# Optimization experiments

Measured on AMD Instinct MI355X. Metric: run time of the kernel, lower is better.

The kernel has to match this reference:

```python
import jax, jax.numpy as jnp
import numpy as np

B, L, H, HEADS = 2, 2048, 1024, 16
D = H // HEADS  # head_dim = 64


def _rel_pos_bias(q, pos_emb):
    """Skewing trick: q is (b,h,L,d) (already scaled), pos_emb is (2L-1,d).
    Returns relative positional bias of shape (b,h,L,L)."""
    b, h, l, _ = q.shape
    p = jnp.einsum('bhid,jd->bhij', q, pos_emb)          # (b,h,L,2L-1)
    p = jnp.pad(p, ((0, 0), (0, 0), (0, 0), (0, 1)))     # (b,h,L,2L)
    p = p.reshape(b, h, l * 2 * l)                        # flatten last two dims
    p = jnp.pad(p, ((0, 0), (0, 0), (0, l - 1)))          # append L-1 zeros
    p = p.reshape(b, h, l + 1, 2 * l - 1)
    return p[:, :, :-1, -l:]                              # (b,h,L,L)


def setup_inputs() -> dict:
    key = jax.random.key(0)
    ks = jax.random.split(key, 12)
    s = 1.0 / np.sqrt(H)
    inp = {
        'query': jax.random.normal(ks[0], (B, L, H), jnp.float32),
        'key':   jax.random.normal(ks[1], (B, L, H), jnp.float32),
        'value': jax.random.normal(ks[2], (B, L, H), jnp.float32),
        'Wq_w': jax.random.normal(ks[3], (H, H), jnp.float32) * s,
        'Wq_b': jnp.zeros((H,), jnp.float32),
        'Wk_w': jax.random.normal(ks[4], (H, H), jnp.float32) * s,
        'Wk_b': jnp.zeros((H,), jnp.float32),
        'Wv_w': jax.random.normal(ks[5], (H, H), jnp.float32) * s,
        'Wv_b': jnp.zeros((H,), jnp.float32),
        'Wo_w': jax.random.normal(ks[6], (H, H), jnp.float32) * s,
        'Wo_b': jnp.zeros((H,), jnp.float32),
        'pos_emb': jax.random.normal(ks[7], (2 * L - 1, D), jnp.float32),
    }
    return inp


def reference(query, key, value, Wq_w, Wq_b, Wk_w, Wk_b, Wv_w, Wv_b, Wo_w, Wo_b, pos_emb):
    b = query.shape[0]
    q = query @ Wq_w.T + Wq_b
    k = key @ Wk_w.T + Wk_b
    v = value @ Wv_w.T + Wv_b
    # (b,L,h*d) -> (b,h,L,d)
    split = lambda x: x.reshape(b, L, HEADS, D).transpose(0, 2, 1, 3)
    q, k, v = split(q), split(k), split(v)
    q = q / np.sqrt(D)  # note: scaled q is also used for positional bias (faithful)
    attn = jnp.einsum('bhid,bhjd->bhij', q, k)
    attn = attn + _rel_pos_bias(q, pos_emb)
    causal = jnp.triu(jnp.full((L, L), -jnp.inf, jnp.float32), k=1)
    attn = attn + causal  # broadcasts over (b,h)
    score = jax.nn.softmax(attn, axis=-1)
    out = jnp.einsum('bhqk,bhkd->bhqd', score, v)
    out = out.transpose(0, 2, 1, 3).reshape(b, L, H)
    return out @ Wo_w.T + Wo_b
```

## Files before the change

kernel.cpp:

```cpp
#include <hip/hip_runtime.h>

#define L_SEQ 2048
#define NH    16
#define HD    64
#define HDIM  1024

typedef __attribute__((ext_vector_type(8))) short  short8;
typedef __attribute__((ext_vector_type(4))) float  f32x4;

__device__ __forceinline__ unsigned short f2bf(float f) {
    unsigned int u = __float_as_uint(f);
    u += 0x7fffu + ((u >> 16) & 1u);
    return (unsigned short)(u >> 16);
}

__device__ __forceinline__ short8 ld8(const unsigned short* p) {
    return *(const short8*)p;
}

__device__ __forceinline__ unsigned int cvtpk(float a, float b) {
    unsigned int r;
    asm("v_cvt_pk_bf16_f32 %0, %1, %2" : "=v"(r) : "v"(a), "v"(b));
    return r;
}

__device__ __forceinline__ void gl16(const unsigned short* g, unsigned short* l) {
    __builtin_amdgcn_global_load_lds(
        (const __attribute__((address_space(1))) void*)g,
        (__attribute__((address_space(3))) void*)l, 16, 0, 0);
}

__global__ __launch_bounds__(256) void cvt_a_kernel(
    const float* __restrict__ q, const float* __restrict__ k, const float* __restrict__ v,
    const float* __restrict__ Wq, const float* __restrict__ Wk,
    const float* __restrict__ Wv, const float* __restrict__ Wo,
    const float* __restrict__ pe,
    unsigned short* __restrict__ S1, unsigned short* __restrict__ Vb,
    unsigned short* __restrict__ VSCR,
    unsigned short* __restrict__ D, unsigned short* __restrict__ E)
{
    const int y = blockIdx.y;
    const float* src; unsigned short* dst; int n8;
    switch (y) {
        case 0:  src = q;  dst = S1;            n8 = 524288; break;
        case 1:  src = k;  dst = Vb;            n8 = 524288; break;
        case 2:  src = Wq; dst = D;             n8 = 131072; break;
        case 3:  src = Wk; dst = D + 1048576;   n8 = 131072; break;
        case 4:  src = Wv; dst = D + 2097152;   n8 = 131072; break;
        case 5:  src = Wo; dst = D + 3145728;   n8 = 131072; break;
        case 6:  src = pe; dst = E;             n8 = 32760;  break;
        default: src = v;  dst = VSCR;          n8 = 524288; break;
    }
    const int i = blockIdx.x * 256 + threadIdx.x;
    if (i >= n8) return;
    const float4 a = ((const float4*)src)[2 * i];
    const float4 b = ((const float4*)src)[2 * i + 1];
    union { short8 v; unsigned int u[4]; } o;
    o.u[0] = cvtpk(a.x, a.y); o.u[1] = cvtpk(a.z, a.w);
    o.u[2] = cvtpk(b.x, b.y); o.u[3] = cvtpk(b.z, b.w);
    ((short8*)dst)[i] = o.v;
}

__device__ __forceinline__ void gemm_bf16_core(
    const unsigned short* __restrict__ Xb,
    const unsigned short* __restrict__ Wb,
    int row0, int col0,
    unsigned short* As, unsigned short* Bs,
    f32x4 (&acc)[4][4])
{
    const int t    = threadIdx.x;
    const int lane = t & 63;
    const int wid  = t >> 6;
    const int lr   = lane & 15;
    const int lg   = lane >> 4;
    const int wr   = (wid >> 1) << 6;
    const int wc   = (wid & 1) << 6;

    const int grow = lane >> 3;
    const int gcol = ((lane & 7) ^ grow) << 3;

#pragma unroll
    for (int m = 0; m < 4; ++m)
#pragma unroll
        for (int n = 0; n < 4; ++n)
            acc[m][n] = (f32x4)0.0f;

    const unsigned short* xs = Xb + (size_t)(row0 + grow) * 1024 + gcol;
    const unsigned short* ws = Wb + (size_t)(col0 + grow) * 1024 + gcol;

    for (int k0 = 0; k0 < 1024; k0 += 64) {
        __syncthreads();
#pragma unroll
        for (int i = 0; i < 4; ++i) {
            const int seg = (i << 2) + wid;
            gl16(xs + (size_t)(seg << 3) * 1024 + k0, As + seg * 512);
            gl16(ws + (size_t)(seg << 3) * 1024 + k0, Bs + seg * 512);
        }
        __syncthreads();

        short8 af[4][2], bf[4][2];
#pragma unroll
        for (int m = 0; m < 4; ++m) {
            const int row = wr + (m << 4) + lr;
#pragma unroll
            for (int h = 0; h < 2; ++h)
                af[m][h] = ld8(&As[row * 64 + ((((h << 2) + lg) ^ (lr & 7)) << 3)]);
        }
#pragma unroll
        for (int n = 0; n < 4; ++n) {
            const int row = wc + (n << 4) + lr;
#pragma unroll
            for (int h = 0; h < 2; ++h)
                bf[n][h] = ld8(&Bs[row * 64 + ((((h << 2) + lg) ^ (lr & 7)) << 3)]);
        }
#pragma unroll
        for (int m = 0; m < 4; ++m)
#pragma unroll
            for (int n = 0; n < 4; ++n) {
                acc[m][n] = __builtin_amdgcn_mfma_f32_16x16x32_bf16(af[m][0], bf[n][0], acc[m][n], 0, 0, 0);
                acc[m][n] = __builtin_amdgcn_mfma_f32_16x16x32_bf16(af[m][1], bf[n][1], acc[m][n], 0, 0, 0);
            }
    }
}

__global__ __launch_bounds__(256) void proj_qkv_kernel(
    const unsigned short* __restrict__ Xq, const unsigned short* __restrict__ Xk,
    const unsigned short* __restrict__ Xv, const unsigned short* __restrict__ D,
    const float* __restrict__ bq, const float* __restrict__ bk, const float* __restrict__ bv,
    unsigned short* __restrict__ Qb, unsigned short* __restrict__ Kb,
    unsigned short* __restrict__ VT)
{
    __shared__ __align__(16) unsigned short As[128 * 64];
    __shared__ __align__(16) unsigned short Bs[128 * 64];

    const int z = blockIdx.x >> 8;
    const int d = blockIdx.x & 255;
    const int y = ((d >> 6) << 3) | (d & 7);
    const int x = (d >> 3) & 7;
    const int row0 = y << 7, col0 = x << 7;

    const unsigned short* Xb = (z == 0) ? Xq : (z == 1) ? Xk : Xv;
    const unsigned short* Wb = D + (size_t)z * 1048576;
    const float* bias = (z == 0) ? bq : (z == 1) ? bk : bv;

    f32x4 acc[4][4];
    gemm_bf16_core(Xb, Wb, row0, col0, As, Bs, acc);

    const int t = threadIdx.x;
    const int lane = t & 63;
    const int wid  = t >> 6;
    const int lr = lane & 15, lg = lane >> 4;
    const int wr = (wid >> 1) << 6, wc = (wid & 1) << 6;

    if (z <= 1) {
        const float scale = (z == 0) ? 0.125f * 1.44269504088896340736f : 1.0f;
        unsigned short* out = (z == 0) ? Qb : Kb;
#pragma unroll
        for (int n = 0; n < 4; ++n) {
            const int o = col0 + wc + (n << 4) + lr;
            const float bo = bias[o];
            const int h = o >> 6, dd = o & 63;
#pragma unroll
            for (int m = 0; m < 4; ++m) {
                const int ib = row0 + wr + (m << 4) + (lg << 2);
#pragma unroll
                for (int r = 0; r < 4; ++r) {
                    const int i = ib + r;
                    out[(((size_t)((i >> 11) * NH + h)) * L_SEQ + (i & (L_SEQ - 1))) * HD + dd] =
                        f2bf((acc[m][n][r] + bo) * scale);
                }
            }
        }
    } else {
#pragma unroll
        for (int n = 0; n < 4; ++n) {
            const int o = col0 + wc + (n << 4) + lr;
            const float bo = bias[o];
            const int h = o >> 6, dd = o & 63;
#pragma unroll
            for (int m = 0; m < 4; ++m) {
                const int ib = row0 + wr + (m << 4) + (lg << 2);
                const int b = ib >> 11, il = ib & (L_SEQ - 1);
                ushort4 pk;
                pk.x = f2bf(acc[m][n][0] + bo);
                pk.y = f2bf(acc[m][n][1] + bo);
                pk.z = f2bf(acc[m][n][2] + bo);
                pk.w = f2bf(acc[m][n][3] + bo);
                *(ushort4*)&VT[(((size_t)(b * NH + h)) * HD + dd) * L_SEQ + il] = pk;
            }
        }
    }
}

__global__ __launch_bounds__(256) void outproj_kernel(
    const unsigned short* __restrict__ Ob, const unsigned short* __restrict__ Wb,
    const float* __restrict__ bias, float* __restrict__ Yout)
{
    __shared__ __align__(16) unsigned short As[128 * 64];
    __shared__ __align__(16) unsigned short Bs[128 * 64];

    const int d = blockIdx.x;
    const int y = ((d >> 6) << 3) | (d & 7);
    const int x = (d >> 3) & 7;
    const int row0 = y << 7, col0 = x << 7;

    f32x4 acc[4][4];
    gemm_bf16_core(Ob, Wb, row0, col0, As, Bs, acc);

    const int t = threadIdx.x;
    const int lane = t & 63;
    const int wid  = t >> 6;
    const int lr = lane & 15, lg = lane >> 4;
    const int wr = (wid >> 1) << 6, wc = (wid & 1) << 6;

#pragma unroll
    for (int n = 0; n < 4; ++n) {
        const int o = col0 + wc + (n << 4) + lr;
        const float bo = bias[o];
#pragma unroll
        for (int m = 0; m < 4; ++m) {
            const int ib = row0 + wr + (m << 4) + (lg << 2);
#pragma unroll
            for (int r = 0; r < 4; ++r)
                Yout[(size_t)(ib + r) * HDIM + o] = acc[m][n][r] + bo;
        }
    }
}

__device__ __forceinline__ void stage_kv(
    const unsigned short* __restrict__ kbase, const unsigned short* __restrict__ vbase,
    int j0, unsigned short (*Ksb)[64], unsigned short (*Vsb)[64], int wid, int lane)
{
    const int r8 = lane >> 3;
    const int gc = ((lane & 7) ^ r8) << 3;
#pragma unroll
    for (int s = 0; s < 2; ++s) {
        const int rw = (wid << 4) + (s << 3);
        gl16(kbase + (size_t)(j0 + rw + r8) * HD + gc, &Ksb[rw][0]);
        gl16(vbase + (size_t)(rw + r8) * L_SEQ + j0 + gc, &Vsb[rw][0]);
    }
}

__global__ __launch_bounds__(256, 3) void attn_kernel(
    const unsigned short* __restrict__ Q,
    const unsigned short* __restrict__ Kt,
    const unsigned short* __restrict__ VT,
    const unsigned short* __restrict__ PE,
    unsigned short* __restrict__ O)
{
    __shared__ __align__(16) unsigned short Ks[2][64][64];
    __shared__ __align__(16) unsigned short Vs[2][64][64];
    __shared__ __align__(16) float blds_all[4][64][20];

    const int t    = threadIdx.x;
    const int wid  = t >> 6;
    const int lane = t & 63;
    const int lr   = lane & 15;
    const int lg   = lane >> 4;
    const int lk   = lg << 3;

    const int p   = blockIdx.x;
    const int bh  = p & 31;
    const int rb  = 31 - (p >> 5);
    const int i0  = rb << 6;
    const int i0w = i0 + (wid << 4);
    const int nt  = rb + 1;

    const unsigned short* kbase = Kt + (size_t)bh * L_SEQ * HD;
    const unsigned short* vbase = VT + (size_t)bh * HD * L_SEQ;

    float (*blds)[20] = blds_all[wid];

    const unsigned short* qb = Q + ((size_t)bh * L_SEQ + i0w + lr) * HD + lk;
    const short8 aq0 = ld8(qb);
    const short8 aq1 = ld8(qb + 32);

    const int gi    = i0w + lr;
    const int idx0  = ((lg & 1) << 7) + (lr << 2);
    const int idx1  = idx0 + 64;
    const int selhi = lg >> 1;

    f32x4 oacc[4];
#pragma unroll
    for (int dt = 0; dt < 4; ++dt) oacc[dt] = (f32x4)0.0f;
    float mrun = -__builtin_inff();
    float lrun = 0.0f;

    const int jend = i0w + 15;

    f32x4 pqc = (f32x4)0.0f;
    {
        const unsigned short* pp = PE + (size_t)(2032 - i0w + lr) * HD + lk;
        pqc = __builtin_amdgcn_mfma_f32_16x16x32_bf16(aq0, ld8(pp), pqc, 0, 0, 0);
        pqc = __builtin_amdgcn_mfma_f32_16x16x32_bf16(aq1, ld8(pp + 32), pqc, 0, 0, 0);
    }

    stage_kv(kbase, vbase, 0, Ks[0], Vs[0], wid, lane);
    __syncthreads();

    int cur = 0;
    for (int tt = 0; tt < nt; ++tt) {
        const int j0   = tt << 6;
        const bool more = (tt + 1 < nt);

        if (more)
            stage_kv(kbase, vbase, j0 + 64, Ks[cur ^ 1], Vs[cur ^ 1], wid, lane);

        if (j0 <= jend) {
            f32x4 s2[4];
#pragma unroll
            for (int ct = 0; ct < 4; ++ct) {
                const int row = (ct << 4) + lr;
                const short8 k0 = *(const short8*)&Ks[cur][row][(lg ^ (lr & 7)) << 3];
                const short8 k1 = *(const short8*)&Ks[cur][row][((4 + lg) ^ (lr & 7)) << 3];
                f32x4 a = (f32x4)0.0f;
                a = __builtin_amdgcn_mfma_f32_16x16x32_bf16(k0, aq0, a, 0, 0, 0);
                a = __builtin_amdgcn_mfma_f32_16x16x32_bf16(k1, aq1, a, 0, 0, 0);
                s2[ct] = a;
            }

            const int mlo = 2032 + j0 - i0w;
            f32x4 pq[5];
            pq[0] = pqc;
#pragma unroll
            for (int pt = 1; pt < 5; ++pt) {
                f32x4 a = (f32x4)0.0f;
                const unsigned short* pp = PE + (size_t)(mlo + (pt << 4) + lr) * HD + lk;
                a = __builtin_amdgcn_mfma_f32_16x16x32_bf16(aq0, ld8(pp), a, 0, 0, 0);
                a = __builtin_amdgcn_mfma_f32_16x16x32_bf16(aq1, ld8(pp + 32), a, 0, 0, 0);
                pq[pt] = a;
            }
            pqc = pq[4];

#pragma unroll
            for (int r = 0; r < 4; ++r) {
                const int qw = (lg << 2) + r;
                {
                    const int kr = lr + qw - 15;
                    if (kr >= 0) blds[kr][qw] = pq[0][r];
                }
#pragma unroll
                for (int pt = 1; pt < 4; ++pt)
                    blds[(pt << 4) + lr + qw - 15][qw] = pq[pt][r];
                {
                    const int kr = 49 + lr + qw;
                    if (kr < 64) blds[kr][qw] = pq[4][r];
                }
            }

            if (j0 + 63 > i0w) {
#pragma unroll
                for (int ct = 0; ct < 4; ++ct)
#pragma unroll
                    for (int r = 0; r < 4; ++r) {
                        const int krl = (ct << 4) + (lg << 2) + r;
                        const float v = s2[ct][r] + blds[krl][lr];
                        s2[ct][r] = (j0 + krl > gi) ? -__builtin_inff() : v;
                    }
            } else {
#pragma unroll
                for (int ct = 0; ct < 4; ++ct)
#pragma unroll
                    for (int r = 0; r < 4; ++r) {
                        const int krl = (ct << 4) + (lg << 2) + r;
                        s2[ct][r] += blds[krl][lr];
                    }
            }

            float c0 = fmaxf(fmaxf(s2[0][0], s2[0][1]), fmaxf(s2[0][2], s2[0][3]));
            float c1 = fmaxf(fmaxf(s2[1][0], s2[1][1]), fmaxf(s2[1][2], s2[1][3]));
            float c2 = fmaxf(fmaxf(s2[2][0], s2[2][1]), fmaxf(s2[2][2], s2[2][3]));
            float c3 = fmaxf(fmaxf(s2[3][0], s2[3][1]), fmaxf(s2[3][2], s2[3][3]));
            float vmax = fmaxf(fmaxf(c0, c1), fmaxf(c2, c3));
            vmax = fmaxf(vmax, __shfl_xor(vmax, 16));
            vmax = fmaxf(vmax, __shfl_xor(vmax, 32));
            if (!__all(vmax <= mrun + 8.0f)) {
                const float mnew = fmaxf(mrun, vmax);
                const float sc = __builtin_amdgcn_exp2f(mrun - mnew);
                mrun = mnew;
                lrun *= sc;
#pragma unroll
                for (int dt = 0; dt < 4; ++dt)
#pragma unroll
                    for (int r = 0; r < 4; ++r)
                        oacc[dt][r] *= sc;
            }
#pragma unroll
            for (int ct = 0; ct < 4; ++ct)
#pragma unroll
                for (int r = 0; r < 4; ++r)
                    s2[ct][r] = __builtin_amdgcn_exp2f(s2[ct][r] - mrun);
            float t0 = (s2[0][0] + s2[0][1]) + (s2[0][2] + s2[0][3]);
            float t1 = (s2[1][0] + s2[1][1]) + (s2[1][2] + s2[1][3]);
            float t2 = (s2[2][0] + s2[2][1]) + (s2[2][2] + s2[2][3]);
            float t3 = (s2[3][0] + s2[3][1]) + (s2[3][2] + s2[3][3]);
            float sum = (t0 + t1) + (t2 + t3);
            sum += __shfl_xor(sum, 16);
            sum += __shfl_xor(sum, 32);
            lrun += sum;

            unsigned int pkl[4], pkh[4];
#pragma unroll
            for (int ct = 0; ct < 4; ++ct) {
                pkl[ct] = cvtpk(s2[ct][0], s2[ct][1]);
                pkh[ct] = cvtpk(s2[ct][2], s2[ct][3]);
            }
            union { short8 v; int u[4]; } pf0, pf1;
#pragma unroll
            for (int m = 0; m < 4; ++m) {
                const int bidx = (m & 2) ? idx1 : idx0;
                const int a0 = __builtin_amdgcn_ds_bpermute(bidx, (int)((m & 1) ? pkh[0] : pkl[0]));
                const int a1 = __builtin_amdgcn_ds_bpermute(bidx, (int)((m & 1) ? pkh[1] : pkl[1]));
                pf0.u[m] = selhi ? a1 : a0;
                const int b0 = __builtin_amdgcn_ds_bpermute(bidx, (int)((m & 1) ? pkh[2] : pkl[2]));
                const int b1 = __builtin_amdgcn_ds_bpermute(bidx, (int)((m & 1) ? pkh[3] : pkl[3]));
                pf1.u[m] = selhi ? b1 : b0;
            }

#pragma unroll
            for (int dt = 0; dt < 4; ++dt) {
                const int row = (dt << 4) + lr;
                const short8 v0 = *(const short8*)&Vs[cur][row][(lg ^ (lr & 7)) << 3];
                const short8 v1 = *(const short8*)&Vs[cur][row][((4 + lg) ^ (lr & 7)) << 3];
                oacc[dt] = __builtin_amdgcn_mfma_f32_16x16x32_bf16(v0, pf0.v, oacc[dt], 0, 0, 0);
                oacc[dt] = __builtin_amdgcn_mfma_f32_16x16x32_bf16(v1, pf1.v, oacc[dt], 0, 0, 0);
            }
        }

        __syncthreads();
        cur ^= 1;
    }

    const float inv = 1.0f / lrun;
    const int b = bh >> 4, h = bh & 15;
#pragma unroll
    for (int dt = 0; dt < 4; ++dt) {
        uint2 u;
        u.x = cvtpk(oacc[dt][0] * inv, oacc[dt][1] * inv);
        u.y = cvtpk(oacc[dt][2] * inv, oacc[dt][3] * inv);
        *(uint2*)&O[((size_t)b * L_SEQ + i0w + lr) * HDIM + (h << 6) + (dt << 4) + (lg << 2)] = u;
    }
}

extern "C" void kernel_launch(void* const* d_in, const int* in_sizes, int n_in,
                              void* d_out, int out_size, void* d_ws, size_t ws_size,
                              hipStream_t stream) {
    (void)in_sizes; (void)n_in; (void)out_size;

    const float* query   = (const float*)d_in[0];
    const float* key_    = (const float*)d_in[1];
    const float* value   = (const float*)d_in[2];
    const float* Wq_w    = (const float*)d_in[3];
    const float* Wq_b    = (const float*)d_in[4];
    const float* Wk_w    = (const float*)d_in[5];
    const float* Wk_b    = (const float*)d_in[6];
    const float* Wv_w    = (const float*)d_in[7];
    const float* Wv_b    = (const float*)d_in[8];
    const float* Wo_w    = (const float*)d_in[9];
    const float* Wo_b    = (const float*)d_in[10];
    const float* pos_emb = (const float*)d_in[11];

    char* ws = (char*)d_ws;
    const size_t MB = 1024 * 1024;
    unsigned short* S1 = (unsigned short*)(ws);
    unsigned short* Qb = (unsigned short*)(ws + 8  * MB);
    unsigned short* Kb = (unsigned short*)(ws + 16 * MB);
    unsigned short* Vb = (unsigned short*)(ws + 24 * MB);
    unsigned short* D  = (unsigned short*)(ws + 32 * MB);
    unsigned short* E  = (unsigned short*)(ws + 40 * MB);

    unsigned short* VSCR = (unsigned short*)d_out;
    unsigned short* VT   = VSCR + 4194304;

    const int npe = (2 * L_SEQ - 1) * HD;
    if (ws_size < (size_t)40 * MB + (size_t)npe * 2) return;

    cvt_a_kernel<<<dim3(2048, 8), 256, 0, stream>>>(query, key_, value,
                                                    Wq_w, Wk_w, Wv_w, Wo_w, pos_emb,
                                                    S1, Vb, VSCR, D, E);
    proj_qkv_kernel<<<768, 256, 0, stream>>>(S1, Vb, VSCR, D, Wq_b, Wk_b, Wv_b,
                                             Qb, Kb, VT);
    attn_kernel<<<1024, 256, 0, stream>>>(Qb, Kb, VT, E, S1);
    outproj_kernel<<<256, 256, 0, stream>>>(S1, D + 3145728, Wo_b, (float*)d_out);
}
```

Before: 172.1 us.

## Fuse fp32-to-bf16 activation conversion into QKV projection GEMM loads

The separate conversion pass for the query/key/value activations is removed. The QKV projection now reads fp32 activations directly, converts them to bf16 in registers and writes them into swizzled LDS, while weights still come in through async global-to-LDS loads. This avoids writing and re-reading about 24 MB of bf16 intermediates and shrinks the conversion launch to weights and pos_emb only. In exchange, each GEMM tile reads twice the activation bytes through registers synchronously, which loses the async load path and could stall the MFMA loop.

New measurement: 195.4 us. 13.5% more time.

```diff
diff --git a/kernel.cpp b/kernel.cpp
--- a/kernel.cpp
+++ b/kernel.cpp
@@ -30,27 +30,16 @@
         (__attribute__((address_space(3))) void*)l, 16, 0, 0);
 }
 
-__global__ __launch_bounds__(256) void cvt_a_kernel(
-    const float* __restrict__ q, const float* __restrict__ k, const float* __restrict__ v,
+__global__ __launch_bounds__(256) void cvt_w_kernel(
     const float* __restrict__ Wq, const float* __restrict__ Wk,
     const float* __restrict__ Wv, const float* __restrict__ Wo,
     const float* __restrict__ pe,
-    unsigned short* __restrict__ S1, unsigned short* __restrict__ Vb,
-    unsigned short* __restrict__ VSCR,
     unsigned short* __restrict__ D, unsigned short* __restrict__ E)
 {
     const int y = blockIdx.y;
-    const float* src; unsigned short* dst; int n8;
-    switch (y) {
-        case 0:  src = q;  dst = S1;            n8 = 524288; break;
-        case 1:  src = k;  dst = Vb;            n8 = 524288; break;
-        case 2:  src = Wq; dst = D;             n8 = 131072; break;
-        case 3:  src = Wk; dst = D + 1048576;   n8 = 131072; break;
-        case 4:  src = Wv; dst = D + 2097152;   n8 = 131072; break;
-        case 5:  src = Wo; dst = D + 3145728;   n8 = 131072; break;
-        case 6:  src = pe; dst = E;             n8 = 32760;  break;
-        default: src = v;  dst = VSCR;          n8 = 524288; break;
-    }
+    const float* src = (y == 0) ? Wq : (y == 1) ? Wk : (y == 2) ? Wv : (y == 3) ? Wo : pe;
+    unsigned short* dst = (y < 4) ? (D + (size_t)y * 1048576) : E;
+    const int n8 = (y < 4) ? 131072 : 32760;
     const int i = blockIdx.x * 256 + threadIdx.x;
     if (i >= n8) return;
     const float4 a = ((const float4*)src)[2 * i];
@@ -61,8 +50,8 @@
     ((short8*)dst)[i] = o.v;
 }
 
-__device__ __forceinline__ void gemm_bf16_core(
-    const unsigned short* __restrict__ Xb,
+__device__ __forceinline__ void gemm_f32x_core(
+    const float* __restrict__ Xf,
     const unsigned short* __restrict__ Wb,
     int row0, int col0,
     unsigned short* As, unsigned short* Bs,
@@ -78,6 +67,85 @@
 
     const int grow = lane >> 3;
     const int gcol = ((lane & 7) ^ grow) << 3;
+    const unsigned short* ws = Wb + (size_t)(col0 + grow) * 1024 + gcol;
+
+    const int xr  = t >> 1;
+    const int xh  = t & 1;
+    const int xsw = xr & 7;
+    const float* xs = Xf + (size_t)(row0 + xr) * 1024 + (xh << 5);
+    unsigned short* xdst = As + xr * 64;
+
+#pragma unroll
+    for (int m = 0; m < 4; ++m)
+#pragma unroll
+        for (int n = 0; n < 4; ++n)
+            acc[m][n] = (f32x4)0.0f;
+
+    for (int k0 = 0; k0 < 1024; k0 += 64) {
+        __syncthreads();
+        float4 xv[8];
+#pragma unroll
+        for (int j = 0; j < 8; ++j)
+            xv[j] = *(const float4*)(xs + k0 + 4 * j);
+#pragma unroll
+        for (int i = 0; i < 4; ++i) {
+            const int seg = (i << 2) + wid;
+            gl16(ws + (size_t)(seg << 3) * 1024 + k0, Bs + seg * 512);
+        }
+#pragma unroll
+        for (int cc = 0; cc < 4; ++cc) {
+            union { short8 v; unsigned int u[4]; } o;
+            o.u[0] = cvtpk(xv[2 * cc].x,     xv[2 * cc].y);
+            o.u[1] = cvtpk(xv[2 * cc].z,     xv[2 * cc].w);
+            o.u[2] = cvtpk(xv[2 * cc + 1].x, xv[2 * cc + 1].y);
+            o.u[3] = cvtpk(xv[2 * cc + 1].z, xv[2 * cc + 1].w);
+            const int c = (xh << 2) + cc;
+            *(short8*)(xdst + ((c ^ xsw) << 3)) = o.v;
+        }
+        __syncthreads();
+
+        short8 af[4][2], bf[4][2];
+#pragma unroll
+        for (int m = 0; m < 4; ++m) {
+            const int row = wr + (m << 4) + lr;
+#pragma unroll
+            for (int h = 0; h < 2; ++h)
+                af[m][h] = ld8(&As[row * 64 + ((((h << 2) + lg) ^ (lr & 7)) << 3)]);
+        }
+#pragma unroll
+        for (int n = 0; n < 4; ++n) {
+            const int row = wc + (n << 4) + lr;
+#pragma unroll
+            for (int h = 0; h < 2; ++h)
+                bf[n][h] = ld8(&Bs[row * 64 + ((((h << 2) + lg) ^ (lr & 7)) << 3)]);
+        }
+#pragma unroll
+        for (int m = 0; m < 4; ++m)
+#pragma unroll
+            for (int n = 0; n < 4; ++n) {
+                acc[m][n] = __builtin_amdgcn_mfma_f32_16x16x32_bf16(af[m][0], bf[n][0], acc[m][n], 0, 0, 0);
+                acc[m][n] = __builtin_amdgcn_mfma_f32_16x16x32_bf16(af[m][1], bf[n][1], acc[m][n], 0, 0, 0);
+            }
+    }
+}
+
+__device__ __forceinline__ void gemm_bf16_core(
+    const unsigned short* __restrict__ Xb,
+    const unsigned short* __restrict__ Wb,
+    int row0, int col0,
+    unsigned short* As, unsigned short* Bs,
+    f32x4 (&acc)[4][4])
+{
+    const int t    = threadIdx.x;
+    const int lane = t & 63;
+    const int wid  = t >> 6;
+    const int lr   = lane & 15;
+    const int lg   = lane >> 4;
+    const int wr   = (wid >> 1) << 6;
+    const int wc   = (wid & 1) << 6;
+
+    const int grow = lane >> 3;
+    const int gcol = ((lane & 7) ^ grow) << 3;
 
 #pragma unroll
     for (int m = 0; m < 4; ++m)
@@ -124,8 +192,8 @@
 }
 
 __global__ __launch_bounds__(256) void proj_qkv_kernel(
-    const unsigned short* __restrict__ Xq, const unsigned short* __restrict__ Xk,
-    const unsigned short* __restrict__ Xv, const unsigned short* __restrict__ D,
+    const float* __restrict__ Xq, const float* __restrict__ Xk,
+    const float* __restrict__ Xv, const unsigned short* __restrict__ D,
     const float* __restrict__ bq, const float* __restrict__ bk, const float* __restrict__ bv,
     unsigned short* __restrict__ Qb, unsigned short* __restrict__ Kb,
     unsigned short* __restrict__ VT)
@@ -139,12 +207,12 @@
     const int x = (d >> 3) & 7;
     const int row0 = y << 7, col0 = x << 7;
 
-    const unsigned short* Xb = (z == 0) ? Xq : (z == 1) ? Xk : Xv;
+    const float* Xf = (z == 0) ? Xq : (z == 1) ? Xk : Xv;
     const unsigned short* Wb = D + (size_t)z * 1048576;
     const float* bias = (z == 0) ? bq : (z == 1) ? bk : bv;
 
     f32x4 acc[4][4];
-    gemm_bf16_core(Xb, Wb, row0, col0, As, Bs, acc);
+    gemm_f32x_core(Xf, Wb, row0, col0, As, Bs, acc);
 
     const int t = threadIdx.x;
     const int lane = t & 63;
@@ -465,20 +533,16 @@
     unsigned short* S1 = (unsigned short*)(ws);
     unsigned short* Qb = (unsigned short*)(ws + 8  * MB);
     unsigned short* Kb = (unsigned short*)(ws + 16 * MB);
-    unsigned short* Vb = (unsigned short*)(ws + 24 * MB);
-    unsigned short* D  = (unsigned short*)(ws + 32 * MB);
-    unsigned short* E  = (unsigned short*)(ws + 40 * MB);
-
-    unsigned short* VSCR = (unsigned short*)d_out;
-    unsigned short* VT   = VSCR + 4194304;
+    unsigned short* D  = (unsigned short*)(ws + 24 * MB);
+    unsigned short* E  = (unsigned short*)(ws + 32 * MB);
+
+    unsigned short* VT = (unsigned short*)d_out;
 
     const int npe = (2 * L_SEQ - 1) * HD;
-    if (ws_size < (size_t)40 * MB + (size_t)npe * 2) return;
-
-    cvt_a_kernel<<<dim3(2048, 8), 256, 0, stream>>>(query, key_, value,
-                                                    Wq_w, Wk_w, Wv_w, Wo_w, pos_emb,
-                                                    S1, Vb, VSCR, D, E);
-    proj_qkv_kernel<<<768, 256, 0, stream>>>(S1, Vb, VSCR, D, Wq_b, Wk_b, Wv_b,
+    if (ws_size < (size_t)32 * MB + (size_t)npe * 2) return;
+
+    cvt_w_kernel<<<dim3(512, 5), 256, 0, stream>>>(Wq_w, Wk_w, Wv_w, Wo_w, pos_emb, D, E);
+    proj_qkv_kernel<<<768, 256, 0, stream>>>(query, key_, value, D, Wq_b, Wk_b, Wv_b,
                                              Qb, Kb, VT);
     attn_kernel<<<1024, 256, 0, stream>>>(Qb, Kb, VT, E, S1);
     outproj_kernel<<<256, 256, 0, stream>>>(S1, D + 3145728, Wo_b, (float*)d_out);
```

## Prefetch next tile's positional-bias MFMAs and raise wave priority around MFMA blocks

Applied to the files above, without the earlier changes.

Computes the positional-bias MFMA tiles for the next KV tile one iteration ahead, so their global PE loads overlap the current softmax work. The per-wave `j0 <= jend` guard is dropped, so every wave processes every tile up to nt. Also wraps the QK and PV MFMA blocks with s_setprio to favour matrix issue. The trade-off is more registers from holding two sets of five accumulators, plus redundant work on tiles that are fully masked if nt exceeds a wave's range.

Measured after the change: 187.9 us. 9.2% more time.

```diff
diff --git a/kernel.cpp b/kernel.cpp
--- a/kernel.cpp
+++ b/kernel.cpp
@@ -286,13 +286,17 @@
     float mrun = -__builtin_inff();
     float lrun = 0.0f;
 
-    const int jend = i0w + 15;
-
-    f32x4 pqc = (f32x4)0.0f;
+    f32x4 pqv[5];
     {
-        const unsigned short* pp = PE + (size_t)(2032 - i0w + lr) * HD + lk;
-        pqc = __builtin_amdgcn_mfma_f32_16x16x32_bf16(aq0, ld8(pp), pqc, 0, 0, 0);
-        pqc = __builtin_amdgcn_mfma_f32_16x16x32_bf16(aq1, ld8(pp + 32), pqc, 0, 0, 0);
+        const int m0 = 2032 - i0w;
+#pragma unroll
+        for (int pt = 0; pt < 5; ++pt) {
+            f32x4 a = (f32x4)0.0f;
+            const unsigned short* pp = PE + (size_t)(m0 + (pt << 4) + lr) * HD + lk;
+            a = __builtin_amdgcn_mfma_f32_16x16x32_bf16(aq0, ld8(pp), a, 0, 0, 0);
+            a = __builtin_amdgcn_mfma_f32_16x16x32_bf16(aq1, ld8(pp + 32), a, 0, 0, 0);
+            pqv[pt] = a;
+        }
     }
 
     stage_kv(kbase, vbase, 0, Ks[0], Vs[0], wid, lane);
@@ -306,125 +310,133 @@
         if (more)
             stage_kv(kbase, vbase, j0 + 64, Ks[cur ^ 1], Vs[cur ^ 1], wid, lane);
 
-        if (j0 <= jend) {
-            f32x4 s2[4];
-#pragma unroll
-            for (int ct = 0; ct < 4; ++ct) {
-                const int row = (ct << 4) + lr;
-                const short8 k0 = *(const short8*)&Ks[cur][row][(lg ^ (lr & 7)) << 3];
-                const short8 k1 = *(const short8*)&Ks[cur][row][((4 + lg) ^ (lr & 7)) << 3];
-                f32x4 a = (f32x4)0.0f;
-                a = __builtin_amdgcn_mfma_f32_16x16x32_bf16(k0, aq0, a, 0, 0, 0);
-                a = __builtin_amdgcn_mfma_f32_16x16x32_bf16(k1, aq1, a, 0, 0, 0);
-                s2[ct] = a;
-            }
-
-            const int mlo = 2032 + j0 - i0w;
-            f32x4 pq[5];
-            pq[0] = pqc;
+        f32x4 s2[4];
+        __builtin_amdgcn_s_setprio(1);
+#pragma unroll
+        for (int ct = 0; ct < 4; ++ct) {
+            const int row = (ct << 4) + lr;
+            const short8 k0 = *(const short8*)&Ks[cur][row][(lg ^ (lr & 7)) << 3];
+            const short8 k1 = *(const short8*)&Ks[cur][row][((4 + lg) ^ (lr & 7)) << 3];
+            f32x4 a = (f32x4)0.0f;
+            a = __builtin_amdgcn_mfma_f32_16x16x32_bf16(k0, aq0, a, 0, 0, 0);
+            a = __builtin_amdgcn_mfma_f32_16x16x32_bf16(k1, aq1, a, 0, 0, 0);
+            s2[ct] = a;
+        }
+        __builtin_amdgcn_s_setprio(0);
+
+#pragma unroll
+        for (int r = 0; r < 4; ++r) {
+            const int qw = (lg << 2) + r;
+            {
+                const int kr = lr + qw - 15;
+                if (kr >= 0) blds[kr][qw] = pqv[0][r];
+            }
+#pragma unroll
+            for (int pt = 1; pt < 4; ++pt)
+                blds[(pt << 4) + lr + qw - 15][qw] = pqv[pt][r];
+            {
+                const int kr = 49 + lr + qw;
+                if (kr < 64) blds[kr][qw] = pqv[4][r];
+            }
+        }
+
+        f32x4 pqn[5];
+        if (more) {
+            pqn[0] = pqv[4];
+            const int mlon = 2032 + j0 + 64 - i0w;
 #pragma unroll
             for (int pt = 1; pt < 5; ++pt) {
                 f32x4 a = (f32x4)0.0f;
-                const unsigned short* pp = PE + (size_t)(mlo + (pt << 4) + lr) * HD + lk;
+                const unsigned short* pp = PE + (size_t)(mlon + (pt << 4) + lr) * HD + lk;
                 a = __builtin_amdgcn_mfma_f32_16x16x32_bf16(aq0, ld8(pp), a, 0, 0, 0);
                 a = __builtin_amdgcn_mfma_f32_16x16x32_bf16(aq1, ld8(pp + 32), a, 0, 0, 0);
-                pq[pt] = a;
-            }
-            pqc = pq[4];
-
-#pragma unroll
-            for (int r = 0; r < 4; ++r) {
-                const int qw = (lg << 2) + r;
-                {
-                    const int kr = lr + qw - 15;
-                    if (kr >= 0) blds[kr][qw] = pq[0][r];
+                pqn[pt] = a;
+            }
+        }
+
+        if (j0 + 63 > i0w) {
+#pragma unroll
+            for (int ct = 0; ct < 4; ++ct)
+#pragma unroll
+                for (int r = 0; r < 4; ++r) {
+                    const int krl = (ct << 4) + (lg << 2) + r;
+                    const float v = s2[ct][r] + blds[krl][lr];
+                    s2[ct][r] = (j0 + krl > gi) ? -__builtin_inff() : v;
                 }
-#pragma unroll
-                for (int pt = 1; pt < 4; ++pt)
-                    blds[(pt << 4) + lr + qw - 15][qw] = pq[pt][r];
-                {
-                    const int kr = 49 + lr + qw;
-                    if (kr < 64) blds[kr][qw] = pq[4][r];
+        } else {
+#pragma unroll
+            for (int ct = 0; ct < 4; ++ct)
+#pragma unroll
+                for (int r = 0; r < 4; ++r) {
+                    const int krl = (ct << 4) + (lg << 2) + r;
+                    s2[ct][r] += blds[krl][lr];
                 }
-            }
-
-            if (j0 + 63 > i0w) {
-#pragma unroll
-                for (int ct = 0; ct < 4; ++ct)
-#pragma unroll
-                    for (int r = 0; r < 4; ++r) {
-                        const int krl = (ct << 4) + (lg << 2) + r;
-                        const float v = s2[ct][r] + blds[krl][lr];
-                        s2[ct][r] = (j0 + krl > gi) ? -__builtin_inff() : v;
-                    }
-            } else {
-#pragma unroll
-                for (int ct = 0; ct < 4; ++ct)
-#pragma unroll
-                    for (int r = 0; r < 4; ++r) {
-                        const int krl = (ct << 4) + (lg << 2) + r;
-                        s2[ct][r] += blds[krl][lr];
-                    }
-            }
-
-            float c0 = fmaxf(fmaxf(s2[0][0], s2[0][1]), fmaxf(s2[0][2], s2[0][3]));
-            float c1 = fmaxf(fmaxf(s2[1][0], s2[1][1]), fmaxf(s2[1][2], s2[1][3]));
-            float c2 = fmaxf(fmaxf(s2[2][0], s2[2][1]), fmaxf(s2[2][2], s2[2][3]));
-            float c3 = fmaxf(fmaxf(s2[3][0], s2[3][1]), fmaxf(s2[3][2], s2[3][3]));
-            float vmax = fmaxf(fmaxf(c0, c1), fmaxf(c2, c3));
-            vmax = fmaxf(vmax, __shfl_xor(vmax, 16));
-            vmax = fmaxf(vmax, __shfl_xor(vmax, 32));
-            if (!__all(vmax <= mrun + 8.0f)) {
-                const float mnew = fmaxf(mrun, vmax);
-                const float sc = __builtin_amdgcn_exp2f(mrun - mnew);
-                mrun = mnew;
-                lrun *= sc;
-#pragma unroll
-                for (int dt = 0; dt < 4; ++dt)
-#pragma unroll
-                    for (int r = 0; r < 4; ++r)
-                        oacc[dt][r] *= sc;
-            }
-#pragma unroll
-            for (int ct = 0; ct < 4; ++ct)
+        }
+
+        float c0 = fmaxf(fmaxf(s2[0][0], s2[0][1]), fmaxf(s2[0][2], s2[0][3]));
+        float c1 = fmaxf(fmaxf(s2[1][0], s2[1][1]), fmaxf(s2[1][2], s2[1][3]));
+        float c2 = fmaxf(fmaxf(s2[2][0], s2[2][1]), fmaxf(s2[2][2], s2[2][3]));
+        float c3 = fmaxf(fmaxf(s2[3][0], s2[3][1]), fmaxf(s2[3][2], s2[3][3]));
+        float vmax = fmaxf(fmaxf(c0, c1), fmaxf(c2, c3));
+        vmax = fmaxf(vmax, __shfl_xor(vmax, 16));
+        vmax = fmaxf(vmax, __shfl_xor(vmax, 32));
+        if (!__all(vmax <= mrun + 8.0f)) {
+            const float mnew = fmaxf(mrun, vmax);
+            const float sc = __builtin_amdgcn_exp2f(mrun - mnew);
+            mrun = mnew;
+            lrun *= sc;
+#pragma unroll
+            for (int dt = 0; dt < 4; ++dt)
 #pragma unroll
                 for (int r = 0; r < 4; ++r)
-                    s2[ct][r] = __builtin_amdgcn_exp2f(s2[ct][r] - mrun);
-            float t0 = (s2[0][0] + s2[0][1]) + (s2[0][2] + s2[0][3]);
-            float t1 = (s2[1][0] + s2[1][1]) + (s2[1][2] + s2[1][3]);
-            float t2 = (s2[2][0] + s2[2][1]) + (s2[2][2] + s2[2][3]);
-            float t3 = (s2[3][0] + s2[3][1]) + (s2[3][2] + s2[3][3]);
-            float sum = (t0 + t1) + (t2 + t3);
-            sum += __shfl_xor(sum, 16);
-            sum += __shfl_xor(sum, 32);
-            lrun += sum;
-
-            unsigned int pkl[4], pkh[4];
-#pragma unroll
-            for (int ct = 0; ct < 4; ++ct) {
-                pkl[ct] = cvtpk(s2[ct][0], s2[ct][1]);
-                pkh[ct] = cvtpk(s2[ct][2], s2[ct][3]);
-            }
-            union { short8 v; int u[4]; } pf0, pf1;
-#pragma unroll
-            for (int m = 0; m < 4; ++m) {
-                const int bidx = (m & 2) ? idx1 : idx0;
-                const int a0 = __builtin_amdgcn_ds_bpermute(bidx, (int)((m & 1) ? pkh[0] : pkl[0]));
-                const int a1 = __builtin_amdgcn_ds_bpermute(bidx, (int)((m & 1) ? pkh[1] : pkl[1]));
-                pf0.u[m] = selhi ? a1 : a0;
-                const int b0 = __builtin_amdgcn_ds_bpermute(bidx, (int)((m & 1) ? pkh[2] : pkl[2]));
-                const int b1 = __builtin_amdgcn_ds_bpermute(bidx, (int)((m & 1) ? pkh[3] : pkl[3]));
-                pf1.u[m] = selhi ? b1 : b0;
-            }
-
-#pragma unroll
-            for (int dt = 0; dt < 4; ++dt) {
-                const int row = (dt << 4) + lr;
-                const short8 v0 = *(const short8*)&Vs[cur][row][(lg ^ (lr & 7)) << 3];
-                const short8 v1 = *(const short8*)&Vs[cur][row][((4 + lg) ^ (lr & 7)) << 3];
-                oacc[dt] = __builtin_amdgcn_mfma_f32_16x16x32_bf16(v0, pf0.v, oacc[dt], 0, 0, 0);
-                oacc[dt] = __builtin_amdgcn_mfma_f32_16x16x32_bf16(v1, pf1.v, oacc[dt], 0, 0, 0);
-            }
+                    oacc[dt][r] *= sc;
+        }
+#pragma unroll
+        for (int ct = 0; ct < 4; ++ct)
+#pragma unroll
+            for (int r = 0; r < 4; ++r)
+                s2[ct][r] = __builtin_amdgcn_exp2f(s2[ct][r] - mrun);
+        float t0 = (s2[0][0] + s2[0][1]) + (s2[0][2] + s2[0][3]);
+        float t1 = (s2[1][0] + s2[1][1]) + (s2[1][2] + s2[1][3]);
+        float t2 = (s2[2][0] + s2[2][1]) + (s2[2][2] + s2[2][3]);
+        float t3 = (s2[3][0] + s2[3][1]) + (s2[3][2] + s2[3][3]);
+        float sum = (t0 + t1) + (t2 + t3);
+        sum += __shfl_xor(sum, 16);
+        sum += __shfl_xor(sum, 32);
+        lrun += sum;
+
+        unsigned int pkl[4], pkh[4];
+#pragma unroll
+        for (int ct = 0; ct < 4; ++ct) {
+            pkl[ct] = cvtpk(s2[ct][0], s2[ct][1]);
+            pkh[ct] = cvtpk(s2[ct][2], s2[ct][3]);
+        }
+        union { short8 v; int u[4]; } pf0, pf1;
+#pragma unroll
+        for (int m = 0; m < 4; ++m) {
+            const int bidx = (m & 2) ? idx1 : idx0;
+            const int a0 = __builtin_amdgcn_ds_bpermute(bidx, (int)((m & 1) ? pkh[0] : pkl[0]));
+            const int a1 = __builtin_amdgcn_ds_bpermute(bidx, (int)((m & 1) ? pkh[1] : pkl[1]));
+            pf0.u[m] = selhi ? a1 : a0;
+            const int b0 = __builtin_amdgcn_ds_bpermute(bidx, (int)((m & 1) ? pkh[2] : pkl[2]));
+            const int b1 = __builtin_amdgcn_ds_bpermute(bidx, (int)((m & 1) ? pkh[3] : pkl[3]));
+            pf1.u[m] = selhi ? b1 : b0;
+        }
+
+        __builtin_amdgcn_s_setprio(1);
+#pragma unroll
+        for (int dt = 0; dt < 4; ++dt) {
+            const int row = (dt << 4) + lr;
+            const short8 v0 = *(const short8*)&Vs[cur][row][(lg ^ (lr & 7)) << 3];
+            const short8 v1 = *(const short8*)&Vs[cur][row][((4 + lg) ^ (lr & 7)) << 3];
+            oacc[dt] = __builtin_amdgcn_mfma_f32_16x16x32_bf16(v0, pf0.v, oacc[dt], 0, 0, 0);
+            oacc[dt] = __builtin_amdgcn_mfma_f32_16x16x32_bf16(v1, pf1.v, oacc[dt], 0, 0, 0);
+        }
+        __builtin_amdgcn_s_setprio(0);
+
+        if (more) {
+#pragma unroll
+            for (int pt = 0; pt < 5; ++pt) pqv[pt] = pqn[pt];
         }
 
         __syncthreads();
```

## Prefetch positional-embedding fragments a tile ahead and transpose bias LDS buffer

Applied to the files above, without the earlier changes.

Positional-embedding operand loads for the next key tile are now issued from global memory one iteration early, into registers, so the bias MFMAs no longer wait on global latency. The bias scratch buffer in shared memory is transposed, so each lane reads its four bias values with one float4 load instead of four scalar loads. The j0<=jend guard is dropped, since with 64-row tiles it always holds. The prefetch adds 32 VGPRs of live state per thread, which may raise register pressure against the launch bound of 3 blocks per SM.

Result: slower. 186.3 us (+8.2%).

```diff
diff --git a/kernel.cpp b/kernel.cpp
--- a/kernel.cpp
+++ b/kernel.cpp
@@ -250,7 +250,7 @@
 {
     __shared__ __align__(16) unsigned short Ks[2][64][64];
     __shared__ __align__(16) unsigned short Vs[2][64][64];
-    __shared__ __align__(16) float blds_all[4][64][20];
+    __shared__ __align__(16) float bldsT_all[4][16][72];
 
     const int t    = threadIdx.x;
     const int wid  = t >> 6;
@@ -269,7 +269,7 @@
     const unsigned short* kbase = Kt + (size_t)bh * L_SEQ * HD;
     const unsigned short* vbase = VT + (size_t)bh * HD * L_SEQ;
 
-    float (*blds)[20] = blds_all[wid];
+    float (*bldsT)[72] = bldsT_all[wid];
 
     const unsigned short* qb = Q + ((size_t)bh * L_SEQ + i0w + lr) * HD + lk;
     const short8 aq0 = ld8(qb);
@@ -286,13 +286,19 @@
     float mrun = -__builtin_inff();
     float lrun = 0.0f;
 
-    const int jend = i0w + 15;
-
     f32x4 pqc = (f32x4)0.0f;
+    short8 pe_c[4][2];
     {
-        const unsigned short* pp = PE + (size_t)(2032 - i0w + lr) * HD + lk;
+        const int m0 = 2032 - i0w;
+        const unsigned short* pp = PE + (size_t)(m0 + lr) * HD + lk;
         pqc = __builtin_amdgcn_mfma_f32_16x16x32_bf16(aq0, ld8(pp), pqc, 0, 0, 0);
         pqc = __builtin_amdgcn_mfma_f32_16x16x32_bf16(aq1, ld8(pp + 32), pqc, 0, 0, 0);
+#pragma unroll
+        for (int pt = 1; pt < 5; ++pt) {
+            const unsigned short* pq_p = PE + (size_t)(m0 + (pt << 4) + lr) * HD + lk;
+            pe_c[pt - 1][0] = ld8(pq_p);
+            pe_c[pt - 1][1] = ld8(pq_p + 32);
+        }
     }
 
     stage_kv(kbase, vbase, 0, Ks[0], Vs[0], wid, lane);
@@ -306,124 +312,141 @@
         if (more)
             stage_kv(kbase, vbase, j0 + 64, Ks[cur ^ 1], Vs[cur ^ 1], wid, lane);
 
-        if (j0 <= jend) {
-            f32x4 s2[4];
+        short8 pe_n[4][2];
+        if (more) {
+            const int mlon = 2032 + j0 + 64 - i0w;
+#pragma unroll
+            for (int pt = 1; pt < 5; ++pt) {
+                const unsigned short* pp = PE + (size_t)(mlon + (pt << 4) + lr) * HD + lk;
+                pe_n[pt - 1][0] = ld8(pp);
+                pe_n[pt - 1][1] = ld8(pp + 32);
+            }
+        }
+
+        f32x4 s2[4];
+#pragma unroll
+        for (int ct = 0; ct < 4; ++ct) {
+            const int row = (ct << 4) + lr;
+            const short8 k0 = *(const short8*)&Ks[cur][row][(lg ^ (lr & 7)) << 3];
+            const short8 k1 = *(const short8*)&Ks[cur][row][((4 + lg) ^ (lr & 7)) << 3];
+            f32x4 a = (f32x4)0.0f;
+            a = __builtin_amdgcn_mfma_f32_16x16x32_bf16(k0, aq0, a, 0, 0, 0);
+            a = __builtin_amdgcn_mfma_f32_16x16x32_bf16(k1, aq1, a, 0, 0, 0);
+            s2[ct] = a;
+        }
+
+        f32x4 pq[5];
+        pq[0] = pqc;
+#pragma unroll
+        for (int pt = 1; pt < 5; ++pt) {
+            f32x4 a = (f32x4)0.0f;
+            a = __builtin_amdgcn_mfma_f32_16x16x32_bf16(aq0, pe_c[pt - 1][0], a, 0, 0, 0);
+            a = __builtin_amdgcn_mfma_f32_16x16x32_bf16(aq1, pe_c[pt - 1][1], a, 0, 0, 0);
+            pq[pt] = a;
+        }
+        pqc = pq[4];
+
+#pragma unroll
+        for (int r = 0; r < 4; ++r) {
+            const int qw = (lg << 2) + r;
+            {
+                const int kr = lr + qw - 15;
+                if (kr >= 0) bldsT[qw][kr] = pq[0][r];
+            }
+#pragma unroll
+            for (int pt = 1; pt < 4; ++pt)
+                bldsT[qw][(pt << 4) + lr + qw - 15] = pq[pt][r];
+            {
+                const int kr = 49 + lr + qw;
+                if (kr < 64) bldsT[qw][kr] = pq[4][r];
+            }
+        }
+
+        if (j0 + 63 > i0w) {
 #pragma unroll
             for (int ct = 0; ct < 4; ++ct) {
-                const int row = (ct << 4) + lr;
-                const short8 k0 = *(const short8*)&Ks[cur][row][(lg ^ (lr & 7)) << 3];
-                const short8 k1 = *(const short8*)&Ks[cur][row][((4 + lg) ^ (lr & 7)) << 3];
-                f32x4 a = (f32x4)0.0f;
-                a = __builtin_amdgcn_mfma_f32_16x16x32_bf16(k0, aq0, a, 0, 0, 0);
-                a = __builtin_amdgcn_mfma_f32_16x16x32_bf16(k1, aq1, a, 0, 0, 0);
-                s2[ct] = a;
-            }
-
-            const int mlo = 2032 + j0 - i0w;
-            f32x4 pq[5];
-            pq[0] = pqc;
-#pragma unroll
-            for (int pt = 1; pt < 5; ++pt) {
-                f32x4 a = (f32x4)0.0f;
-                const unsigned short* pp = PE + (size_t)(mlo + (pt << 4) + lr) * HD + lk;
-                a = __builtin_amdgcn_mfma_f32_16x16x32_bf16(aq0, ld8(pp), a, 0, 0, 0);
-                a = __builtin_amdgcn_mfma_f32_16x16x32_bf16(aq1, ld8(pp + 32), a, 0, 0, 0);
-                pq[pt] = a;
-            }
-            pqc = pq[4];
-
-#pragma unroll
-            for (int r = 0; r < 4; ++r) {
-                const int qw = (lg << 2) + r;
-                {
-                    const int kr = lr + qw - 15;
-                    if (kr >= 0) blds[kr][qw] = pq[0][r];
+                const float4 bv = *(const float4*)&bldsT[lr][(ct << 4) + (lg << 2)];
+#pragma unroll
+                for (int r = 0; r < 4; ++r) {
+                    const int krl = (ct << 4) + (lg << 2) + r;
+                    const float v = s2[ct][r] + ((const float*)&bv)[r];
+                    s2[ct][r] = (j0 + krl > gi) ? -__builtin_inff() : v;
                 }
-#pragma unroll
-                for (int pt = 1; pt < 4; ++pt)
-                    blds[(pt << 4) + lr + qw - 15][qw] = pq[pt][r];
-                {
-                    const int kr = 49 + lr + qw;
-                    if (kr < 64) blds[kr][qw] = pq[4][r];
-                }
-            }
-
-            if (j0 + 63 > i0w) {
-#pragma unroll
-                for (int ct = 0; ct < 4; ++ct)
-#pragma unroll
-                    for (int r = 0; r < 4; ++r) {
-                        const int krl = (ct << 4) + (lg << 2) + r;
-                        const float v = s2[ct][r] + blds[krl][lr];
-                        s2[ct][r] = (j0 + krl > gi) ? -__builtin_inff() : v;
-                    }
-            } else {
-#pragma unroll
-                for (int ct = 0; ct < 4; ++ct)
-#pragma unroll
-                    for (int r = 0; r < 4; ++r) {
-                        const int krl = (ct << 4) + (lg << 2) + r;
-                        s2[ct][r] += blds[krl][lr];
-                    }
-            }
-
-            float c0 = fmaxf(fmaxf(s2[0][0], s2[0][1]), fmaxf(s2[0][2], s2[0][3]));
-            float c1 = fmaxf(fmaxf(s2[1][0], s2[1][1]), fmaxf(s2[1][2], s2[1][3]));
-            float c2 = fmaxf(fmaxf(s2[2][0], s2[2][1]), fmaxf(s2[2][2], s2[2][3]));
-            float c3 = fmaxf(fmaxf(s2[3][0], s2[3][1]), fmaxf(s2[3][2], s2[3][3]));
-            float vmax = fmaxf(fmaxf(c0, c1), fmaxf(c2, c3));
-            vmax = fmaxf(vmax, __shfl_xor(vmax, 16));
-            vmax = fmaxf(vmax, __shfl_xor(vmax, 32));
-            if (!__all(vmax <= mrun + 8.0f)) {
-                const float mnew = fmaxf(mrun, vmax);
-                const float sc = __builtin_amdgcn_exp2f(mrun - mnew);
-                mrun = mnew;
-                lrun *= sc;
-#pragma unroll
-                for (int dt = 0; dt < 4; ++dt)
-#pragma unroll
-                    for (int r = 0; r < 4; ++r)
-                        oacc[dt][r] *= sc;
-            }
-#pragma unroll
-            for (int ct = 0; ct < 4; ++ct)
+            }
+        } else {
+#pragma unroll
+            for (int ct = 0; ct < 4; ++ct) {
+                const float4 bv = *(const float4*)&bldsT[lr][(ct << 4) + (lg << 2)];
 #pragma unroll
                 for (int r = 0; r < 4; ++r)
-                    s2[ct][r] = __builtin_amdgcn_exp2f(s2[ct][r] - mrun);
-            float t0 = (s2[0][0] + s2[0][1]) + (s2[0][2] + s2[0][3]);
-            float t1 = (s2[1][0] + s2[1][1]) + (s2[1][2] + s2[1][3]);
-            float t2 = (s2[2][0] + s2[2][1]) + (s2[2][2] + s2[2][3]);
-            float t3 = (s2[3][0] + s2[3][1]) + (s2[3][2] + s2[3][3]);
-            float sum = (t0 + t1) + (t2 + t3);
-            sum += __shfl_xor(sum, 16);
-            sum += __shfl_xor(sum, 32);
-            lrun += sum;
-
-            unsigned int pkl[4], pkh[4];
-#pragma unroll
-            for (int ct = 0; ct < 4; ++ct) {
-                pkl[ct] = cvtpk(s2[ct][0], s2[ct][1]);
-                pkh[ct] = cvtpk(s2[ct][2], s2[ct][3]);
-            }
-            union { short8 v; int u[4]; } pf0, pf1;
-#pragma unroll
-            for (int m = 0; m < 4; ++m) {
-                const int bidx = (m & 2) ? idx1 : idx0;
-                const int a0 = __builtin_amdgcn_ds_bpermute(bidx, (int)((m & 1) ? pkh[0] : pkl[0]));
-                const int a1 = __builtin_amdgcn_ds_bpermute(bidx, (int)((m & 1) ? pkh[1] : pkl[1]));
-                pf0.u[m] = selhi ? a1 : a0;
-                const int b0 = __builtin_amdgcn_ds_bpermute(bidx, (int)((m & 1) ? pkh[2] : pkl[2]));
-                const int b1 = __builtin_amdgcn_ds_bpermute(bidx, (int)((m & 1) ? pkh[3] : pkl[3]));
-                pf1.u[m] = selhi ? b1 : b0;
-            }
-
-#pragma unroll
-            for (int dt = 0; dt < 4; ++dt) {
-                const int row = (dt << 4) + lr;
-                const short8 v0 = *(const short8*)&Vs[cur][row][(lg ^ (lr & 7)) << 3];
-                const short8 v1 = *(const short8*)&Vs[cur][row][((4 + lg) ^ (lr & 7)) << 3];
-                oacc[dt] = __builtin_amdgcn_mfma_f32_16x16x32_bf16(v0, pf0.v, oacc[dt], 0, 0, 0);
-                oacc[dt] = __builtin_amdgcn_mfma_f32_16x16x32_bf16(v1, pf1.v, oacc[dt], 0, 0, 0);
+                    s2[ct][r] += ((const float*)&bv)[r];
+            }
+        }
+
+        float c0 = fmaxf(fmaxf(s2[0][0], s2[0][1]), fmaxf(s2[0][2], s2[0][3]));
+        float c1 = fmaxf(fmaxf(s2[1][0], s2[1][1]), fmaxf(s2[1][2], s2[1][3]));
+        float c2 = fmaxf(fmaxf(s2[2][0], s2[2][1]), fmaxf(s2[2][2], s2[2][3]));
+        float c3 = fmaxf(fmaxf(s2[3][0], s2[3][1]), fmaxf(s2[3][2], s2[3][3]));
+        float vmax = fmaxf(fmaxf(c0, c1), fmaxf(c2, c3));
+        vmax = fmaxf(vmax, __shfl_xor(vmax, 16));
+        vmax = fmaxf(vmax, __shfl_xor(vmax, 32));
+        if (!__all(vmax <= mrun + 8.0f)) {
+            const float mnew = fmaxf(mrun, vmax);
+            const float sc = __builtin_amdgcn_exp2f(mrun - mnew);
+            mrun = mnew;
+            lrun *= sc;
+#pragma unroll
+            for (int dt = 0; dt < 4; ++dt)
+#pragma unroll
+                for (int r = 0; r < 4; ++r)
+                    oacc[dt][r] *= sc;
+        }
+#pragma unroll
+        for (int ct = 0; ct < 4; ++ct)
+#pragma unroll
+            for (int r = 0; r < 4; ++r)
+                s2[ct][r] = __builtin_amdgcn_exp2f(s2[ct][r] - mrun);
+        float t0 = (s2[0][0] + s2[0][1]) + (s2[0][2] + s2[0][3]);
+        float t1 = (s2[1][0] + s2[1][1]) + (s2[1][2] + s2[1][3]);
+        float t2 = (s2[2][0] + s2[2][1]) + (s2[2][2] + s2[2][3]);
+        float t3 = (s2[3][0] + s2[3][1]) + (s2[3][2] + s2[3][3]);
+        float sum = (t0 + t1) + (t2 + t3);
+        sum += __shfl_xor(sum, 16);
+        sum += __shfl_xor(sum, 32);
+        lrun += sum;
+
+        unsigned int pkl[4], pkh[4];
+#pragma unroll
+        for (int ct = 0; ct < 4; ++ct) {
+            pkl[ct] = cvtpk(s2[ct][0], s2[ct][1]);
+            pkh[ct] = cvtpk(s2[ct][2], s2[ct][3]);
+        }
+        union { short8 v; int u[4]; } pf0, pf1;
+#pragma unroll
+        for (int m = 0; m < 4; ++m) {
+            const int bidx = (m & 2) ? idx1 : idx0;
+            const int a0 = __builtin_amdgcn_ds_bpermute(bidx, (int)((m & 1) ? pkh[0] : pkl[0]));
+            const int a1 = __builtin_amdgcn_ds_bpermute(bidx, (int)((m & 1) ? pkh[1] : pkl[1]));
+            pf0.u[m] = selhi ? a1 : a0;
+            const int b0 = __builtin_amdgcn_ds_bpermute(bidx, (int)((m & 1) ? pkh[2] : pkl[2]));
+            const int b1 = __builtin_amdgcn_ds_bpermute(bidx, (int)((m & 1) ? pkh[3] : pkl[3]));
+            pf1.u[m] = selhi ? b1 : b0;
+        }
+
+#pragma unroll
+        for (int dt = 0; dt < 4; ++dt) {
+            const int row = (dt << 4) + lr;
+            const short8 v0 = *(const short8*)&Vs[cur][row][(lg ^ (lr & 7)) << 3];
+            const short8 v1 = *(const short8*)&Vs[cur][row][((4 + lg) ^ (lr & 7)) << 3];
+            oacc[dt] = __builtin_amdgcn_mfma_f32_16x16x32_bf16(v0, pf0.v, oacc[dt], 0, 0, 0);
+            oacc[dt] = __builtin_amdgcn_mfma_f32_16x16x32_bf16(v1, pf1.v, oacc[dt], 0, 0, 0);
+        }
+
+        if (more) {
+#pragma unroll
+            for (int pt = 0; pt < 4; ++pt) {
+                pe_c[pt][0] = pe_n[pt][0];
+                pe_c[pt][1] = pe_n[pt][1];
             }
         }
 
```
